# Kernel optimization log

Measured on AMD Instinct MI355X. Metric: run time of the kernel, lower is better.

Reference implementation:

```python
import jax, jax.numpy as jnp
import numpy as np

N_EMBD = 1024
N_HEADS = 16
HEAD_EMBD = N_EMBD // N_HEADS  # 64
TOTAL = N_HEADS * HEAD_EMBD


def setup_inputs() -> dict:
    key = jax.random.key(0)
    k_x, k_wqkv, k_bqkv, k_wo, k_bo = jax.random.split(key, 5)
    B, S = 2, 2048
    x = jax.random.normal(k_x, (B, S, N_EMBD), dtype=jnp.float32)
    # torch nn.Linear: weight (out, in), y = x @ W.T + b
    lim_qkv = 1.0 / np.sqrt(N_EMBD)
    W_qkv = jax.random.uniform(k_wqkv, (3 * TOTAL, N_EMBD), minval=-lim_qkv, maxval=lim_qkv, dtype=jnp.float32)
    b_qkv = jax.random.uniform(k_bqkv, (3 * TOTAL,), minval=-lim_qkv, maxval=lim_qkv, dtype=jnp.float32)
    lim_o = 1.0 / np.sqrt(TOTAL)
    W_out = jax.random.uniform(k_wo, (N_EMBD, TOTAL), minval=-lim_o, maxval=lim_o, dtype=jnp.float32)
    b_out = jax.random.uniform(k_bo, (N_EMBD,), minval=-lim_o, maxval=lim_o, dtype=jnp.float32)
    return {"x": x, "W_qkv": W_qkv, "b_qkv": b_qkv, "W_out": W_out, "b_out": b_out}


def reference(x, W_qkv, b_qkv, W_out, b_out):
    B, S, _ = x.shape
    qkv = x @ W_qkv.T + b_qkv  # (B, S, 3*H*E)
    # rearrange 'b s (t h e) -> t b h s e'
    qkv = qkv.reshape(B, S, 3, N_HEADS, HEAD_EMBD)
    q = jnp.transpose(qkv[:, :, 0], (0, 2, 1, 3))  # (B, H, S, E)
    k = jnp.transpose(qkv[:, :, 1], (0, 2, 1, 3))
    v = jnp.transpose(qkv[:, :, 2], (0, 2, 1, 3))
    scores = jnp.einsum('bhse,bhte->bhst', q, k) / jnp.sqrt(jnp.float32(HEAD_EMBD))
    # original: tril(scores) + triu(-10000, k=1) == strict-upper entries exactly -10000
    row = jnp.arange(S)[:, None]
    col = jnp.arange(S)[None, :]
    masked = jnp.where(col > row, jnp.float32(-10000.0), scores)
    attn = jax.nn.softmax(masked, axis=-1)  # (B, H, S, S)
    z = jnp.einsum('bhrc,bhce->bhre', attn, v)  # (B, H, S, E)
    z = jnp.transpose(z, (0, 2, 1, 3)).reshape(B, S, TOTAL)
    out = z @ W_out.T + b_out
    return (out, attn)
```

## Files before the change

kernel.cpp:

```cpp
#include <hip/hip_runtime.h>
#include <stdint.h>

typedef __attribute__((ext_vector_type(4))) float f32x4;
typedef __attribute__((ext_vector_type(8))) short short8v;
typedef __attribute__((ext_vector_type(4))) unsigned short ushort4v;

#define DEV __device__ __forceinline__
#define EXP2 __builtin_amdgcn_exp2f
#define WAITVM0 asm volatile("s_waitcnt vmcnt(0)" ::: "memory")
#define WAITVM2 asm volatile("s_waitcnt vmcnt(2)" ::: "memory")
#define WAITVM4 asm volatile("s_waitcnt vmcnt(4)" ::: "memory")
#define FENCE   asm volatile("" ::: "memory")
#define BARRIER __builtin_amdgcn_s_barrier()

DEV unsigned short f2bf(float x) {
    union { float f; uint32_t u; } v; v.f = x;
    uint32_t r = v.u + 0x7fffu + ((v.u >> 16) & 1u);
    return (unsigned short)(r >> 16);
}
DEV float bf2f(unsigned short h) {
    union { uint32_t u; float f; } v; v.u = ((uint32_t)h) << 16;
    return v.f;
}
DEV f32x4 mfma16(short8v a, short8v b, f32x4 c) {
    return __builtin_amdgcn_mfma_f32_16x16x32_bf16(a, b, c, 0, 0, 0);
}
DEV void gload16(const unsigned short* g, unsigned short* l) {
    __builtin_amdgcn_global_load_lds(
        (const __attribute__((address_space(1))) unsigned int*)g,
        (__attribute__((address_space(3))) unsigned int*)l, 16, 0, 0);
}

__global__ void k_cvt(const float* __restrict__ in, unsigned short* __restrict__ out, int n4) {
    int i = blockIdx.x * blockDim.x + threadIdx.x;
    if (i >= n4) return;
    f32x4 v = *(const f32x4*)(in + (size_t)i * 4);
    ushort4v h;
#pragma unroll
    for (int j = 0; j < 4; ++j) h[j] = f2bf(v[j]);
    *(ushort4v*)(out + (size_t)i * 4) = h;
}

__global__ __launch_bounds__(256) void k_gemm_qkv(
    const unsigned short* __restrict__ XB, const unsigned short* __restrict__ WB,
    const float* __restrict__ BIAS, unsigned short* __restrict__ QKVB) {
    const int K = 1024, N = 3072;
    __shared__ unsigned short As[128][40], Bs[128][40];
    int tid = threadIdx.x, lane = tid & 63, w = tid >> 6;
    int bm = blockIdx.x, bn = blockIdx.y;
    int wr = (w >> 1) * 64, wc = (w & 1) * 64;
    int lrow = lane & 15, lseg = lane >> 4;
    f32x4 acc[4][4];
#pragma unroll
    for (int m = 0; m < 4; ++m)
#pragma unroll
        for (int n = 0; n < 4; ++n) acc[m][n] = (f32x4){0.f, 0.f, 0.f, 0.f};

    for (int k0 = 0; k0 < K; k0 += 32) {
#pragma unroll
        for (int i = 0; i < 2; ++i) {
            int chunk = tid + i * 256;
            int row = chunk >> 2, s8 = (chunk & 3) * 8;
            *(short8v*)&As[row][s8] = *(const short8v*)(XB + (size_t)(bm * 128 + row) * K + k0 + s8);
            *(short8v*)&Bs[row][s8] = *(const short8v*)(WB + (size_t)(bn * 128 + row) * K + k0 + s8);
        }
        __syncthreads();
        short8v fa[4], fb[4];
#pragma unroll
        for (int m = 0; m < 4; ++m) {
            fa[m] = *(const short8v*)&As[wr + m * 16 + lrow][lseg * 8];
            fb[m] = *(const short8v*)&Bs[wc + m * 16 + lrow][lseg * 8];
        }
#pragma unroll
        for (int m = 0; m < 4; ++m)
#pragma unroll
            for (int n = 0; n < 4; ++n)
                acc[m][n] = mfma16(fa[m], fb[n], acc[m][n]);
        __syncthreads();
    }
#pragma unroll
    for (int n = 0; n < 4; ++n) {
        int col = bn * 128 + wc + n * 16 + lrow;
        float bv = BIAS[col];
#pragma unroll
        for (int m = 0; m < 4; ++m) {
            int row = bm * 128 + wr + m * 16 + lseg * 4;
#pragma unroll
            for (int i = 0; i < 4; ++i)
                QKVB[(size_t)(row + i) * N + col] = f2bf(acc[m][n][i] + bv);
        }
    }
}

__global__ void k_prep_v(const unsigned short* __restrict__ QKVB, unsigned short* __restrict__ VT) {
    __shared__ unsigned short vt[32][72];
    int bh = blockIdx.y, b = bh >> 4, h = bh & 15;
    int c0 = blockIdx.x * 32;
    int t = threadIdx.x;
    int c = t >> 3, e8 = (t & 7) * 8;
    *(short8v*)&vt[c][e8] =
        *(const short8v*)(QKVB + (size_t)(b * 2048 + c0 + c) * 3072 + 2048 + h * 64 + e8);
    __syncthreads();
    int e = t & 63, cg = t >> 6;
    unsigned short tmp[8];
#pragma unroll
    for (int i = 0; i < 8; ++i) tmp[i] = vt[cg * 8 + i][e];
    *(short8v*)(VT + ((size_t)bh * 64 + e) * 2048 + c0 + cg * 8) = *(short8v*)tmp;
}

__global__ __launch_bounds__(256) void k_attn(
    const unsigned short* __restrict__ QKVB, const unsigned short* __restrict__ VT,
    float* __restrict__ ATTN, unsigned short* __restrict__ Z) {
    __shared__ __align__(16) unsigned short Kt[2][64 * 64];
    __shared__ __align__(16) unsigned short Vt[2][64 * 64];
    __shared__ __align__(16) float Pl[4][16][68];

    const float SCALE = 0.18033688011112042f;
    int blk = blockIdx.x;
    int bh = blk & 31;
    int rt = 31 - (blk >> 5);
    int b = bh >> 4, h = bh & 15;
    int tid = threadIdx.x, lane = tid & 63, w = tid >> 6;
    int lrow = lane & 15, lseg = lane >> 4;
    int r0 = rt * 64 + w * 16;

    short8v qf[2];
    {
        const unsigned short* qp =
            QKVB + (size_t)(b * 2048 + r0 + lrow) * 3072 + h * 64 + lseg * 8;
#pragma unroll
        for (int kc = 0; kc < 2; ++kc) {
            short8v qr = *(const short8v*)(qp + kc * 32);
            short8v qs;
#pragma unroll
            for (int j = 0; j < 8; ++j)
                qs[j] = (short)f2bf(bf2f((unsigned short)qr[j]) * SCALE);
            qf[kc] = qs;
        }
    }

    auto STAGEK = [&](int buf, int t) {
        const size_t kbase = ((size_t)b * 2048 + (size_t)t * 64) * 3072 + 1024 + h * 64;
#pragma unroll
        for (int dr = 0; dr < 2; ++dr) {
            int U = dr * 256 + tid;
            int c = U >> 3, u = U & 7, us = u ^ (c & 7);
            gload16(QKVB + kbase + (size_t)c * 3072 + us * 8,
                    &Kt[buf][(dr * 256 + (tid & ~63)) * 8]);
        }
    };
    auto STAGEV = [&](int buf, int t) {
        const size_t vbase = (size_t)bh * 64 * 2048 + (size_t)t * 64;
#pragma unroll
        for (int dr = 0; dr < 2; ++dr) {
            int U = dr * 256 + tid;
            int e = U >> 3, u = U & 7, us = u ^ (e & 7);
            gload16(VT + vbase + (size_t)e * 2048 + us * 8,
                    &Vt[buf][(dr * 256 + (tid & ~63)) * 8]);
        }
    };

    float ls4[4] = {0.f, 0.f, 0.f, 0.f};
    STAGEK(0, 0);
    for (int t = 0; t <= rt; ++t) {
        if (t < rt) { STAGEK((t + 1) & 1, t + 1); WAITVM2; } else { WAITVM0; }
        BARRIER;
        const unsigned short* kb = Kt[t & 1];
        f32x4 sc[4];
#pragma unroll
        for (int g = 0; g < 4; ++g) sc[g] = (f32x4){0.f, 0.f, 0.f, 0.f};
#pragma unroll
        for (int kc = 0; kc < 2; ++kc) {
            int uoff = (((kc * 4 + lseg) ^ (lrow & 7)) << 3);
#pragma unroll
            for (int g = 0; g < 4; ++g) {
                short8v kf = *(const short8v*)(kb + (g * 16 + lrow) * 64 + uoff);
                sc[g] = mfma16(qf[kc], kf, sc[g]);
            }
        }
        if (t < rt) {
#pragma unroll
            for (int g = 0; g < 4; ++g)
#pragma unroll
                for (int i = 0; i < 4; ++i) ls4[i] += EXP2(sc[g][i]);
        } else {
            int c0 = t * 64;
#pragma unroll
            for (int g = 0; g < 4; ++g)
#pragma unroll
                for (int i = 0; i < 4; ++i) {
                    float sv = (c0 + g * 16 + lrow > r0 + lseg * 4 + i) ? -1e30f : sc[g][i];
                    ls4[i] += EXP2(sv);
                }
        }
        FENCE; BARRIER;
    }
#pragma unroll
    for (int off = 1; off < 16; off <<= 1)
#pragma unroll
        for (int i = 0; i < 4; ++i) ls4[i] += __shfl_xor(ls4[i], off, 64);
    float invl[4];
#pragma unroll
    for (int i = 0; i < 4; ++i) invl[i] = 1.0f / ls4[i];

    float* ab = ATTN + ((size_t)bh * 2048 + r0) * 2048;
    f32x4 zacc[4];
#pragma unroll
    for (int i = 0; i < 4; ++i) zacc[i] = (f32x4){0.f, 0.f, 0.f, 0.f};

    STAGEK(0, 0); STAGEV(0, 0);
    for (int t = 0; t <= rt; ++t) {
        if (t < rt) { STAGEK((t + 1) & 1, t + 1); STAGEV((t + 1) & 1, t + 1); WAITVM4; }
        else { WAITVM0; }
        BARRIER;
        const unsigned short* kb = Kt[t & 1];
        const unsigned short* vb = Vt[t & 1];
        int c0 = t * 64;
        f32x4 sc[4];
#pragma unroll
        for (int g = 0; g < 4; ++g) sc[g] = (f32x4){0.f, 0.f, 0.f, 0.f};
#pragma unroll
        for (int kc = 0; kc < 2; ++kc) {
            int uoff = (((kc * 4 + lseg) ^ (lrow & 7)) << 3);
#pragma unroll
            for (int g = 0; g < 4; ++g) {
                short8v kf = *(const short8v*)(kb + (g * 16 + lrow) * 64 + uoff);
                sc[g] = mfma16(qf[kc], kf, sc[g]);
            }
        }
        if (t < rt) {
#pragma unroll
            for (int g = 0; g < 4; ++g)
#pragma unroll
                for (int i = 0; i < 4; ++i)
                    Pl[w][lseg * 4 + i][g * 16 + lrow] = EXP2(sc[g][i]) * invl[i];
        } else {
#pragma unroll
            for (int g = 0; g < 4; ++g)
#pragma unroll
                for (int i = 0; i < 4; ++i) {
                    float sv = (c0 + g * 16 + lrow > r0 + lseg * 4 + i) ? -1e30f : sc[g][i];
                    Pl[w][lseg * 4 + i][g * 16 + lrow] = EXP2(sv) * invl[i];
                }
        }
        short8v pf[2];
#pragma unroll
        for (int kc = 0; kc < 2; ++kc) {
            f32x4 p0 = *(const f32x4*)&Pl[w][lrow][kc * 32 + lseg * 8];
            f32x4 p1 = *(const f32x4*)&Pl[w][lrow][kc * 32 + lseg * 8 + 4];
            short8v pv;
#pragma unroll
            for (int j = 0; j < 4; ++j) { pv[j] = (short)f2bf(p0[j]); pv[j + 4] = (short)f2bf(p1[j]); }
            pf[kc] = pv;
        }
#pragma unroll
        for (int kc = 0; kc < 2; ++kc) {
            int uoff = (((kc * 4 + lseg) ^ (lrow & 7)) << 3);
#pragma unroll
            for (int et = 0; et < 4; ++et) {
                short8v vf = *(const short8v*)(vb + (et * 16 + lrow) * 64 + uoff);
                zacc[et] = mfma16(pf[kc], vf, zacc[et]);
            }
        }
        {
            int row = lane >> 2, q = lane & 3;
            const float* pr = &Pl[w][row][0];
            float* gp = ab + (size_t)row * 2048 + c0;
#pragma unroll
            for (int r4 = 0; r4 < 4; ++r4) {
                f32x4 v = *(const f32x4*)(pr + q * 4 + r4 * 16);
                *(f32x4*)(gp + q * 4 + r4 * 16) = v;
            }
        }
        FENCE; BARRIER;
    }

#pragma unroll
    for (int et = 0; et < 4; ++et)
#pragma unroll
        for (int i = 0; i < 4; ++i)
            Z[(size_t)(b * 2048 + r0 + lseg * 4 + i) * 1024 + h * 64 + et * 16 + lrow] =
                f2bf(zacc[et][i]);

    int cz = (rt + 1) * 64;
    for (int r = 0; r < 16; ++r) {
        float* rp = ab + (size_t)r * 2048;
        for (int c = cz + (lane << 2); c < 2048; c += 256)
            *(f32x4*)(rp + c) = (f32x4){0.f, 0.f, 0.f, 0.f};
    }
}

__global__ __launch_bounds__(256) void k_gemm_out(
    const unsigned short* __restrict__ ZB, const unsigned short* __restrict__ WOB,
    const float* __restrict__ BIAS, float* __restrict__ OUT) {
    const int K = 1024, N = 1024;
    __shared__ unsigned short As[128][40], Bs[128][40];
    int tid = threadIdx.x, lane = tid & 63, w = tid >> 6;
    int bm = blockIdx.x, bn = blockIdx.y;
    int wr = (w >> 1) * 64, wc = (w & 1) * 64;
    int lrow = lane & 15, lseg = lane >> 4;
    f32x4 acc[4][4];
#pragma unroll
    for (int m = 0; m < 4; ++m)
#pragma unroll
        for (int n = 0; n < 4; ++n) acc[m][n] = (f32x4){0.f, 0.f, 0.f, 0.f};

    for (int k0 = 0; k0 < K; k0 += 32) {
#pragma unroll
        for (int i = 0; i < 2; ++i) {
            int chunk = tid + i * 256;
            int row = chunk >> 2, s8 = (chunk & 3) * 8;
            *(short8v*)&As[row][s8] = *(const short8v*)(ZB + (size_t)(bm * 128 + row) * K + k0 + s8);
            *(short8v*)&Bs[row][s8] = *(const short8v*)(WOB + (size_t)(bn * 128 + row) * K + k0 + s8);
        }
        __syncthreads();
        short8v fa[4], fb[4];
#pragma unroll
        for (int m = 0; m < 4; ++m) {
            fa[m] = *(const short8v*)&As[wr + m * 16 + lrow][lseg * 8];
            fb[m] = *(const short8v*)&Bs[wc + m * 16 + lrow][lseg * 8];
        }
#pragma unroll
        for (int m = 0; m < 4; ++m)
#pragma unroll
            for (int n = 0; n < 4; ++n)
                acc[m][n] = mfma16(fa[m], fb[n], acc[m][n]);
        __syncthreads();
    }
#pragma unroll
    for (int n = 0; n < 4; ++n) {
        int col = bn * 128 + wc + n * 16 + lrow;
        float bv = BIAS[col];
#pragma unroll
        for (int m = 0; m < 4; ++m) {
            int row = bm * 128 + wr + m * 16 + lseg * 4;
#pragma unroll
            for (int i = 0; i < 4; ++i)
                OUT[(size_t)(row + i) * N + col] = acc[m][n][i] + bv;
        }
    }
}

extern "C" void kernel_launch(void* const* d_in, const int* in_sizes, int n_in,
                              void* d_out, int out_size, void* d_ws, size_t ws_size,
                              hipStream_t stream) {
    const float* X    = (const float*)d_in[0];
    const float* Wqkv = (const float*)d_in[1];
    const float* Bqkv = (const float*)d_in[2];
    const float* Wout = (const float*)d_in[3];
    const float* Bout = (const float*)d_in[4];
    float* out  = (float*)d_out;
    float* attn = out + (size_t)4096 * 1024;

    char* ws = (char*)d_ws;
    unsigned short* QKVB = (unsigned short*)ws; ws += (size_t)4096 * 3072 * 2;
    unsigned short* VTp  = (unsigned short*)ws; ws += (size_t)32 * 64 * 2048 * 2;
    unsigned short* ZBp  = (unsigned short*)ws; ws += (size_t)4096 * 1024 * 2;
    unsigned short* XBp  = (unsigned short*)ws; ws += (size_t)4096 * 1024 * 2;
    unsigned short* WQBp = (unsigned short*)ws; ws += (size_t)3072 * 1024 * 2;
    unsigned short* WOBp = (unsigned short*)ws; ws += (size_t)1024 * 1024 * 2;

    k_cvt<<<4096, 256, 0, stream>>>(X, XBp, 4096 * 1024 / 4);
    k_cvt<<<3072, 256, 0, stream>>>(Wqkv, WQBp, 3072 * 1024 / 4);
    k_cvt<<<1024, 256, 0, stream>>>(Wout, WOBp, 1024 * 1024 / 4);
    k_gemm_qkv<<<dim3(32, 24), 256, 0, stream>>>(XBp, WQBp, Bqkv, QKVB);
    k_prep_v<<<dim3(64, 32), 256, 0, stream>>>(QKVB, VTp);
    k_attn<<<1024, 256, 0, stream>>>(QKVB, VTp, attn, ZBp);
    k_gemm_out<<<dim3(32, 8), 256, 0, stream>>>(ZBp, WOBp, Bout, out);
}
```

Before: 265.6 us.

## Double-buffer GEMMs via LDS DMA, widen attention blocks, fuse conversions, nontemporal stores

Moves both GEMMs onto a shared core that stages A/B tiles straight into LDS with global_load_lds and double buffering, so the next tile loads while MFMAs run. The attention kernel now uses 512 threads over 128-row tiles with balanced row-tile ordering, sharing K/V staging across eight waves. Attention-probability stores and the zero fill of the masked upper triangle use nontemporal stores to limit cache pollution. The three fp32-to-bf16 conversion launches become one. Waves whose rows end earlier sit idle in the last tile, and the larger block may lower occupancy.

After: 278.4 us. +4.8%, slower.

```diff
diff --git a/kernel.cpp b/kernel.cpp
--- a/kernel.cpp
+++ b/kernel.cpp
@@ -8,6 +8,7 @@
 #define DEV __device__ __forceinline__
 #define EXP2 __builtin_amdgcn_exp2f
 #define WAITVM0 asm volatile("s_waitcnt vmcnt(0)" ::: "memory")
+#define WAITVM1 asm volatile("s_waitcnt vmcnt(1)" ::: "memory")
 #define WAITVM2 asm volatile("s_waitcnt vmcnt(2)" ::: "memory")
 #define WAITVM4 asm volatile("s_waitcnt vmcnt(4)" ::: "memory")
 #define FENCE   asm volatile("" ::: "memory")
@@ -30,54 +31,79 @@
         (const __attribute__((address_space(1))) unsigned int*)g,
         (__attribute__((address_space(3))) unsigned int*)l, 16, 0, 0);
 }
-
-__global__ void k_cvt(const float* __restrict__ in, unsigned short* __restrict__ out, int n4) {
+DEV void ntstore4(float* p, f32x4 v) { __builtin_nontemporal_store(v, (f32x4*)p); }
+
+__global__ void k_cvt3(const float* __restrict__ a, unsigned short* __restrict__ oa, int na4,
+                       const float* __restrict__ b, unsigned short* __restrict__ ob, int nb4,
+                       const float* __restrict__ c, unsigned short* __restrict__ oc, int nc4) {
     int i = blockIdx.x * blockDim.x + threadIdx.x;
-    if (i >= n4) return;
-    f32x4 v = *(const f32x4*)(in + (size_t)i * 4);
+    const float* in; unsigned short* out; int idx;
+    if (i < na4) { in = a; out = oa; idx = i; }
+    else if (i < na4 + nb4) { in = b; out = ob; idx = i - na4; }
+    else { idx = i - na4 - nb4; if (idx >= nc4) return; in = c; out = oc; }
+    f32x4 v = *(const f32x4*)(in + (size_t)idx * 4);
     ushort4v h;
 #pragma unroll
     for (int j = 0; j < 4; ++j) h[j] = f2bf(v[j]);
-    *(ushort4v*)(out + (size_t)i * 4) = h;
-}
-
-__global__ __launch_bounds__(256) void k_gemm_qkv(
-    const unsigned short* __restrict__ XB, const unsigned short* __restrict__ WB,
-    const float* __restrict__ BIAS, unsigned short* __restrict__ QKVB) {
-    const int K = 1024, N = 3072;
-    __shared__ unsigned short As[128][40], Bs[128][40];
+    *(ushort4v*)(out + (size_t)idx * 4) = h;
+}
+
+template <int KDIM>
+DEV void gemm_core(const unsigned short* __restrict__ APTR,
+                   const unsigned short* __restrict__ BPTR,
+                   f32x4 (&acc)[4][4]) {
+    __shared__ __align__(16) unsigned short As[2][128 * 32], Bs[2][128 * 32];
     int tid = threadIdx.x, lane = tid & 63, w = tid >> 6;
     int bm = blockIdx.x, bn = blockIdx.y;
     int wr = (w >> 1) * 64, wc = (w & 1) * 64;
     int lrow = lane & 15, lseg = lane >> 4;
-    f32x4 acc[4][4];
 #pragma unroll
     for (int m = 0; m < 4; ++m)
 #pragma unroll
         for (int n = 0; n < 4; ++n) acc[m][n] = (f32x4){0.f, 0.f, 0.f, 0.f};
-
-    for (int k0 = 0; k0 < K; k0 += 32) {
+    auto STAGE = [&](int buf, int k0) {
 #pragma unroll
         for (int i = 0; i < 2; ++i) {
-            int chunk = tid + i * 256;
-            int row = chunk >> 2, s8 = (chunk & 3) * 8;
-            *(short8v*)&As[row][s8] = *(const short8v*)(XB + (size_t)(bm * 128 + row) * K + k0 + s8);
-            *(short8v*)&Bs[row][s8] = *(const short8v*)(WB + (size_t)(bn * 128 + row) * K + k0 + s8);
-        }
-        __syncthreads();
+            int ch = i * 256 + tid;
+            int row = ch >> 2, seg = ch & 3;
+            gload16(APTR + (size_t)(bm * 128 + row) * KDIM + k0 + seg * 8,
+                    &As[buf][(i * 256 + (tid & ~63)) * 8]);
+            gload16(BPTR + (size_t)(bn * 128 + row) * KDIM + k0 + seg * 8,
+                    &Bs[buf][(i * 256 + (tid & ~63)) * 8]);
+        }
+    };
+    const int NT = KDIM / 32;
+    STAGE(0, 0);
+    for (int t = 0; t < NT; ++t) {
+        if (t < NT - 1) { STAGE((t + 1) & 1, (t + 1) * 32); WAITVM4; } else WAITVM0;
+        BARRIER;
+        const unsigned short* as = As[t & 1];
+        const unsigned short* bs = Bs[t & 1];
         short8v fa[4], fb[4];
 #pragma unroll
         for (int m = 0; m < 4; ++m) {
-            fa[m] = *(const short8v*)&As[wr + m * 16 + lrow][lseg * 8];
-            fb[m] = *(const short8v*)&Bs[wc + m * 16 + lrow][lseg * 8];
+            fa[m] = *(const short8v*)(as + (wr + m * 16 + lrow) * 32 + lseg * 8);
+            fb[m] = *(const short8v*)(bs + (wc + m * 16 + lrow) * 32 + lseg * 8);
         }
 #pragma unroll
         for (int m = 0; m < 4; ++m)
 #pragma unroll
             for (int n = 0; n < 4; ++n)
                 acc[m][n] = mfma16(fa[m], fb[n], acc[m][n]);
-        __syncthreads();
-    }
+        FENCE; BARRIER;
+    }
+}
+
+__global__ __launch_bounds__(256) void k_gemm_qkv(
+    const unsigned short* __restrict__ XB, const unsigned short* __restrict__ WB,
+    const float* __restrict__ BIAS, unsigned short* __restrict__ QKVB) {
+    f32x4 acc[4][4];
+    gemm_core<1024>(XB, WB, acc);
+    int tid = threadIdx.x, lane = tid & 63, w = tid >> 6;
+    int bm = blockIdx.x, bn = blockIdx.y;
+    int wr = (w >> 1) * 64, wc = (w & 1) * 64;
+    int lrow = lane & 15, lseg = lane >> 4;
+    const int N = 3072;
 #pragma unroll
     for (int n = 0; n < 4; ++n) {
         int col = bn * 128 + wc + n * 16 + lrow;
@@ -88,6 +114,30 @@
 #pragma unroll
             for (int i = 0; i < 4; ++i)
                 QKVB[(size_t)(row + i) * N + col] = f2bf(acc[m][n][i] + bv);
+        }
+    }
+}
+
+__global__ __launch_bounds__(256) void k_gemm_out(
+    const unsigned short* __restrict__ ZB, const unsigned short* __restrict__ WOB,
+    const float* __restrict__ BIAS, float* __restrict__ OUT) {
+    f32x4 acc[4][4];
+    gemm_core<1024>(ZB, WOB, acc);
+    int tid = threadIdx.x, lane = tid & 63, w = tid >> 6;
+    int bm = blockIdx.x, bn = blockIdx.y;
+    int wr = (w >> 1) * 64, wc = (w & 1) * 64;
+    int lrow = lane & 15, lseg = lane >> 4;
+    const int N = 1024;
+#pragma unroll
+    for (int n = 0; n < 4; ++n) {
+        int col = bn * 128 + wc + n * 16 + lrow;
+        float bv = BIAS[col];
+#pragma unroll
+        for (int m = 0; m < 4; ++m) {
+            int row = bm * 128 + wr + m * 16 + lseg * 4;
+#pragma unroll
+            for (int i = 0; i < 4; ++i)
+                OUT[(size_t)(row + i) * N + col] = acc[m][n][i] + bv;
         }
     }
 }
@@ -108,21 +158,24 @@
     *(short8v*)(VT + ((size_t)bh * 64 + e) * 2048 + c0 + cg * 8) = *(short8v*)tmp;
 }
 
-__global__ __launch_bounds__(256) void k_attn(
+__global__ __launch_bounds__(512) void k_attn(
     const unsigned short* __restrict__ QKVB, const unsigned short* __restrict__ VT,
     float* __restrict__ ATTN, unsigned short* __restrict__ Z) {
     __shared__ __align__(16) unsigned short Kt[2][64 * 64];
     __shared__ __align__(16) unsigned short Vt[2][64 * 64];
-    __shared__ __align__(16) float Pl[4][16][68];
+    __shared__ __align__(16) float Pl[8][16][68];
 
     const float SCALE = 0.18033688011112042f;
     int blk = blockIdx.x;
     int bh = blk & 31;
-    int rt = 31 - (blk >> 5);
+    int rtp = blk >> 5;
+    int rt = (rtp < 8) ? (15 - rtp) : (rtp - 8);
     int b = bh >> 4, h = bh & 15;
     int tid = threadIdx.x, lane = tid & 63, w = tid >> 6;
     int lrow = lane & 15, lseg = lane >> 4;
-    int r0 = rt * 64 + w * 16;
+    int r0 = rt * 128 + w * 16;
+    int T = 2 * rt + 2;
+    int Tw = (r0 >> 6) + 1;
 
     short8v qf[2];
     {
@@ -141,57 +194,49 @@
 
     auto STAGEK = [&](int buf, int t) {
         const size_t kbase = ((size_t)b * 2048 + (size_t)t * 64) * 3072 + 1024 + h * 64;
-#pragma unroll
-        for (int dr = 0; dr < 2; ++dr) {
-            int U = dr * 256 + tid;
-            int c = U >> 3, u = U & 7, us = u ^ (c & 7);
-            gload16(QKVB + kbase + (size_t)c * 3072 + us * 8,
-                    &Kt[buf][(dr * 256 + (tid & ~63)) * 8]);
-        }
+        int c = tid >> 3, u = tid & 7, us = u ^ (c & 7);
+        gload16(QKVB + kbase + (size_t)c * 3072 + us * 8, &Kt[buf][(tid & ~63) * 8]);
     };
     auto STAGEV = [&](int buf, int t) {
         const size_t vbase = (size_t)bh * 64 * 2048 + (size_t)t * 64;
-#pragma unroll
-        for (int dr = 0; dr < 2; ++dr) {
-            int U = dr * 256 + tid;
-            int e = U >> 3, u = U & 7, us = u ^ (e & 7);
-            gload16(VT + vbase + (size_t)e * 2048 + us * 8,
-                    &Vt[buf][(dr * 256 + (tid & ~63)) * 8]);
-        }
+        int e = tid >> 3, u = tid & 7, us = u ^ (e & 7);
+        gload16(VT + vbase + (size_t)e * 2048 + us * 8, &Vt[buf][(tid & ~63) * 8]);
     };
 
     float ls4[4] = {0.f, 0.f, 0.f, 0.f};
     STAGEK(0, 0);
-    for (int t = 0; t <= rt; ++t) {
-        if (t < rt) { STAGEK((t + 1) & 1, t + 1); WAITVM2; } else { WAITVM0; }
+    for (int t = 0; t < T; ++t) {
+        if (t < T - 1) { STAGEK((t + 1) & 1, t + 1); WAITVM1; } else WAITVM0;
         BARRIER;
-        const unsigned short* kb = Kt[t & 1];
-        f32x4 sc[4];
-#pragma unroll
-        for (int g = 0; g < 4; ++g) sc[g] = (f32x4){0.f, 0.f, 0.f, 0.f};
-#pragma unroll
-        for (int kc = 0; kc < 2; ++kc) {
-            int uoff = (((kc * 4 + lseg) ^ (lrow & 7)) << 3);
-#pragma unroll
-            for (int g = 0; g < 4; ++g) {
-                short8v kf = *(const short8v*)(kb + (g * 16 + lrow) * 64 + uoff);
-                sc[g] = mfma16(qf[kc], kf, sc[g]);
-            }
-        }
-        if (t < rt) {
-#pragma unroll
-            for (int g = 0; g < 4; ++g)
-#pragma unroll
-                for (int i = 0; i < 4; ++i) ls4[i] += EXP2(sc[g][i]);
-        } else {
-            int c0 = t * 64;
-#pragma unroll
-            for (int g = 0; g < 4; ++g)
-#pragma unroll
-                for (int i = 0; i < 4; ++i) {
-                    float sv = (c0 + g * 16 + lrow > r0 + lseg * 4 + i) ? -1e30f : sc[g][i];
-                    ls4[i] += EXP2(sv);
+        if (t < Tw) {
+            const unsigned short* kb = Kt[t & 1];
+            f32x4 sc[4];
+#pragma unroll
+            for (int g = 0; g < 4; ++g) sc[g] = (f32x4){0.f, 0.f, 0.f, 0.f};
+#pragma unroll
+            for (int kc = 0; kc < 2; ++kc) {
+                int uoff = (((kc * 4 + lseg) ^ (lrow & 7)) << 3);
+#pragma unroll
+                for (int g = 0; g < 4; ++g) {
+                    short8v kf = *(const short8v*)(kb + (g * 16 + lrow) * 64 + uoff);
+                    sc[g] = mfma16(qf[kc], kf, sc[g]);
                 }
+            }
+            if (t < Tw - 1) {
+#pragma unroll
+                for (int g = 0; g < 4; ++g)
+#pragma unroll
+                    for (int i = 0; i < 4; ++i) ls4[i] += EXP2(sc[g][i]);
+            } else {
+                int c0 = t * 64;
+#pragma unroll
+                for (int g = 0; g < 4; ++g)
+#pragma unroll
+                    for (int i = 0; i < 4; ++i) {
+                        float sv = (c0 + g * 16 + lrow > r0 + lseg * 4 + i) ? -1e30f : sc[g][i];
+                        ls4[i] += EXP2(sv);
+                    }
+            }
         }
         FENCE; BARRIER;
     }
@@ -209,67 +254,67 @@
     for (int i = 0; i < 4; ++i) zacc[i] = (f32x4){0.f, 0.f, 0.f, 0.f};
 
     STAGEK(0, 0); STAGEV(0, 0);
-    for (int t = 0; t <= rt; ++t) {
-        if (t < rt) { STAGEK((t + 1) & 1, t + 1); STAGEV((t + 1) & 1, t + 1); WAITVM4; }
-        else { WAITVM0; }
+    for (int t = 0; t < T; ++t) {
+        if (t < T - 1) { STAGEK((t + 1) & 1, t + 1); STAGEV((t + 1) & 1, t + 1); WAITVM2; }
+        else WAITVM0;
         BARRIER;
-        const unsigned short* kb = Kt[t & 1];
-        const unsigned short* vb = Vt[t & 1];
-        int c0 = t * 64;
-        f32x4 sc[4];
-#pragma unroll
-        for (int g = 0; g < 4; ++g) sc[g] = (f32x4){0.f, 0.f, 0.f, 0.f};
-#pragma unroll
-        for (int kc = 0; kc < 2; ++kc) {
-            int uoff = (((kc * 4 + lseg) ^ (lrow & 7)) << 3);
-#pragma unroll
-            for (int g = 0; g < 4; ++g) {
-                short8v kf = *(const short8v*)(kb + (g * 16 + lrow) * 64 + uoff);
-                sc[g] = mfma16(qf[kc], kf, sc[g]);
-            }
-        }
-        if (t < rt) {
-#pragma unroll
-            for (int g = 0; g < 4; ++g)
-#pragma unroll
-                for (int i = 0; i < 4; ++i)
-                    Pl[w][lseg * 4 + i][g * 16 + lrow] = EXP2(sc[g][i]) * invl[i];
-        } else {
-#pragma unroll
-            for (int g = 0; g < 4; ++g)
-#pragma unroll
-                for (int i = 0; i < 4; ++i) {
-                    float sv = (c0 + g * 16 + lrow > r0 + lseg * 4 + i) ? -1e30f : sc[g][i];
-                    Pl[w][lseg * 4 + i][g * 16 + lrow] = EXP2(sv) * invl[i];
+        if (t < Tw) {
+            const unsigned short* kb = Kt[t & 1];
+            const unsigned short* vb = Vt[t & 1];
+            int c0 = t * 64;
+            f32x4 sc[4];
+#pragma unroll
+            for (int g = 0; g < 4; ++g) sc[g] = (f32x4){0.f, 0.f, 0.f, 0.f};
+#pragma unroll
+            for (int kc = 0; kc < 2; ++kc) {
+                int uoff = (((kc * 4 + lseg) ^ (lrow & 7)) << 3);
+#pragma unroll
+                for (int g = 0; g < 4; ++g) {
+                    short8v kf = *(const short8v*)(kb + (g * 16 + lrow) * 64 + uoff);
+                    sc[g] = mfma16(qf[kc], kf, sc[g]);
                 }
-        }
-        short8v pf[2];
-#pragma unroll
-        for (int kc = 0; kc < 2; ++kc) {
-            f32x4 p0 = *(const f32x4*)&Pl[w][lrow][kc * 32 + lseg * 8];
-            f32x4 p1 = *(const f32x4*)&Pl[w][lrow][kc * 32 + lseg * 8 + 4];
-            short8v pv;
-#pragma unroll
-            for (int j = 0; j < 4; ++j) { pv[j] = (short)f2bf(p0[j]); pv[j + 4] = (short)f2bf(p1[j]); }
-            pf[kc] = pv;
-        }
-#pragma unroll
-        for (int kc = 0; kc < 2; ++kc) {
-            int uoff = (((kc * 4 + lseg) ^ (lrow & 7)) << 3);
-#pragma unroll
-            for (int et = 0; et < 4; ++et) {
-                short8v vf = *(const short8v*)(vb + (et * 16 + lrow) * 64 + uoff);
-                zacc[et] = mfma16(pf[kc], vf, zacc[et]);
-            }
-        }
-        {
-            int row = lane >> 2, q = lane & 3;
-            const float* pr = &Pl[w][row][0];
-            float* gp = ab + (size_t)row * 2048 + c0;
-#pragma unroll
-            for (int r4 = 0; r4 < 4; ++r4) {
-                f32x4 v = *(const f32x4*)(pr + q * 4 + r4 * 16);
-                *(f32x4*)(gp + q * 4 + r4 * 16) = v;
+            }
+            if (t < Tw - 1) {
+#pragma unroll
+                for (int g = 0; g < 4; ++g)
+#pragma unroll
+                    for (int i = 0; i < 4; ++i)
+                        Pl[w][lseg * 4 + i][g * 16 + lrow] = EXP2(sc[g][i]) * invl[i];
+            } else {
+#pragma unroll
+                for (int g = 0; g < 4; ++g)
+#pragma unroll
+                    for (int i = 0; i < 4; ++i) {
+                        float sv = (c0 + g * 16 + lrow > r0 + lseg * 4 + i) ? -1e30f : sc[g][i];
+                        Pl[w][lseg * 4 + i][g * 16 + lrow] = EXP2(sv) * invl[i];
+                    }
+            }
+            short8v pf[2];
+#pragma unroll
+            for (int kc = 0; kc < 2; ++kc) {
+                f32x4 p0 = *(const f32x4*)&Pl[w][lrow][kc * 32 + lseg * 8];
+                f32x4 p1 = *(const f32x4*)&Pl[w][lrow][kc * 32 + lseg * 8 + 4];
+                short8v pv;
+#pragma unroll
+                for (int j = 0; j < 4; ++j) { pv[j] = (short)f2bf(p0[j]); pv[j + 4] = (short)f2bf(p1[j]); }
+                pf[kc] = pv;
+            }
+#pragma unroll
+            for (int kc = 0; kc < 2; ++kc) {
+                int uoff = (((kc * 4 + lseg) ^ (lrow & 7)) << 3);
+#pragma unroll
+                for (int et = 0; et < 4; ++et) {
+                    short8v vf = *(const short8v*)(vb + (et * 16 + lrow) * 64 + uoff);
+                    zacc[et] = mfma16(pf[kc], vf, zacc[et]);
+                }
+            }
+            {
+                int row = lane >> 2, q = lane & 3;
+                const float* pr = &Pl[w][row][0];
+                float* gp = ab + (size_t)row * 2048 + c0;
+#pragma unroll
+                for (int r4 = 0; r4 < 4; ++r4)
+                    ntstore4(gp + q * 4 + r4 * 16, *(const f32x4*)(pr + q * 4 + r4 * 16));
             }
         }
         FENCE; BARRIER;
@@ -282,62 +327,12 @@
             Z[(size_t)(b * 2048 + r0 + lseg * 4 + i) * 1024 + h * 64 + et * 16 + lrow] =
                 f2bf(zacc[et][i]);
 
-    int cz = (rt + 1) * 64;
+    int czw = Tw * 64;
+    const f32x4 zz = (f32x4){0.f, 0.f, 0.f, 0.f};
     for (int r = 0; r < 16; ++r) {
         float* rp = ab + (size_t)r * 2048;
-        for (int c = cz + (lane << 2); c < 2048; c += 256)
-            *(f32x4*)(rp + c) = (f32x4){0.f, 0.f, 0.f, 0.f};
-    }
-}
-
-__global__ __launch_bounds__(256) void k_gemm_out(
-    const unsigned short* __restrict__ ZB, const unsigned short* __restrict__ WOB,
-    const float* __restrict__ BIAS, float* __restrict__ OUT) {
-    const int K = 1024, N = 1024;
-    __shared__ unsigned short As[128][40], Bs[128][40];
-    int tid = threadIdx.x, lane = tid & 63, w = tid >> 6;
-    int bm = blockIdx.x, bn = blockIdx.y;
-    int wr = (w >> 1) * 64, wc = (w & 1) * 64;
-    int lrow = lane & 15, lseg = lane >> 4;
-    f32x4 acc[4][4];
-#pragma unroll
-    for (int m = 0; m < 4; ++m)
-#pragma unroll
-        for (int n = 0; n < 4; ++n) acc[m][n] = (f32x4){0.f, 0.f, 0.f, 0.f};
-
-    for (int k0 = 0; k0 < K; k0 += 32) {
-#pragma unroll
-        for (int i = 0; i < 2; ++i) {
-            int chunk = tid + i * 256;
-            int row = chunk >> 2, s8 = (chunk & 3) * 8;
-            *(short8v*)&As[row][s8] = *(const short8v*)(ZB + (size_t)(bm * 128 + row) * K + k0 + s8);
-            *(short8v*)&Bs[row][s8] = *(const short8v*)(WOB + (size_t)(bn * 128 + row) * K + k0 + s8);
-        }
-        __syncthreads();
-        short8v fa[4], fb[4];
-#pragma unroll
-        for (int m = 0; m < 4; ++m) {
-            fa[m] = *(const short8v*)&As[wr + m * 16 + lrow][lseg * 8];
-            fb[m] = *(const short8v*)&Bs[wc + m * 16 + lrow][lseg * 8];
-        }
-#pragma unroll
-        for (int m = 0; m < 4; ++m)
-#pragma unroll
-            for (int n = 0; n < 4; ++n)
-                acc[m][n] = mfma16(fa[m], fb[n], acc[m][n]);
-        __syncthreads();
-    }
-#pragma unroll
-    for (int n = 0; n < 4; ++n) {
-        int col = bn * 128 + wc + n * 16 + lrow;
-        float bv = BIAS[col];
-#pragma unroll
-        for (int m = 0; m < 4; ++m) {
-            int row = bm * 128 + wr + m * 16 + lseg * 4;
-#pragma unroll
-            for (int i = 0; i < 4; ++i)
-                OUT[(size_t)(row + i) * N + col] = acc[m][n][i] + bv;
-        }
+        for (int c = czw + (lane << 2); c < 2048; c += 256)
+            ntstore4(rp + c, zz);
     }
 }
 
@@ -360,11 +355,11 @@
     unsigned short* WQBp = (unsigned short*)ws; ws += (size_t)3072 * 1024 * 2;
     unsigned short* WOBp = (unsigned short*)ws; ws += (size_t)1024 * 1024 * 2;
 
-    k_cvt<<<4096, 256, 0, stream>>>(X, XBp, 4096 * 1024 / 4);
-    k_cvt<<<3072, 256, 0, stream>>>(Wqkv, WQBp, 3072 * 1024 / 4);
-    k_cvt<<<1024, 256, 0, stream>>>(Wout, WOBp, 1024 * 1024 / 4);
+    const int na4 = 4096 * 1024 / 4, nb4 = 3072 * 1024 / 4, nc4 = 1024 * 1024 / 4;
+    k_cvt3<<<(na4 + nb4 + nc4 + 255) / 256, 256, 0, stream>>>(
+        X, XBp, na4, Wqkv, WQBp, nb4, Wout, WOBp, nc4);
     k_gemm_qkv<<<dim3(32, 24), 256, 0, stream>>>(XBp, WQBp, Bqkv, QKVB);
     k_prep_v<<<dim3(64, 32), 256, 0, stream>>>(QKVB, VTp);
-    k_attn<<<1024, 256, 0, stream>>>(QKVB, VTp, attn, ZBp);
+    k_attn<<<512, 512, 0, stream>>>(QKVB, VTp, attn, ZBp);
     k_gemm_out<<<dim3(32, 8), 256, 0, stream>>>(ZBp, WOBp, Bout, out);
 }
```
